# Kernel tuning notes

Measured on AMD Instinct MI355X. Metric: run time of the kernel, lower is better.

## Reference

```python
import jax, jax.numpy as jnp
import numpy as np

N = 128
# maskDD = full 128x128 (all True); maskL = strictly lower triangular.
# torch's M[:, mask] = entries fills True positions in row-major order,
# which matches np.tril_indices / nonzero ordering.
_L_ROWS, _L_COLS = np.tril_indices(N, -1)  # 8128 entries


def setup_inputs() -> dict:
    key = jax.random.key(0)
    k1, k2, k3 = jax.random.split(key, 3)
    B = 2048
    DD_entries = jax.random.normal(k1, (B, N * N), dtype=jnp.float32)
    L_entries = jax.random.normal(k2, (B, _L_ROWS.size), dtype=jnp.float32) * 0.05
    scale = jax.random.uniform(k3, (1,), dtype=jnp.float32, minval=0.1, maxval=0.5)
    return {"DD_entries": DD_entries, "L_entries": L_entries, "scale": scale}


def reference(DD_entries, L_entries, scale):
    B = DD_entries.shape[0]
    dtype = DD_entries.dtype
    # reconstruct_mat with full mask -> plain reshape
    DD = DD_entries.reshape(B, N, N)
    # reconstruct_mat with strictly-lower-triangular mask (scatter), then * scale
    eps = jnp.zeros((B, N, N), dtype=dtype).at[:, _L_ROWS, _L_COLS].set(L_entries)
    L = eps * scale + jnp.eye(N, dtype=dtype)  # epsilon*scale + I
    LL = L @ jnp.swapaxes(L, -1, -2)           # L L^H (real -> L L^T)
    P = LL @ DD                                 # preconditioned matrix [B,N,N]
    S = jnp.linalg.svd(P, compute_uv=False)    # singular values, descending
    cond = S[..., 0] / S[..., -1]
    return jnp.mean(cond, axis=0)
```

## Files before the change

### kernel.cpp

```cpp
#include <hip/hip_runtime.h>

#define N 128
#define PAD2 129
#define NL 8128
#define POWER_IT 10
#define INV_IT 3
#define INV_WAVES 8
#define NTHREADS 1024

#define NDBL (16512 + 128 + 24 + 24 + 16)
#define SMEM_BYTES (NDBL * 8 + 2 * 143 * 16)
#define XI(j) ((j) + ((j) >> 3))

static __device__ __forceinline__ float hashf(unsigned x) {
    x ^= 2747636419u; x *= 2654435769u; x ^= x >> 16;
    x *= 2654435769u; x ^= x >> 16; x *= 2654435769u;
    return ((float)(x >> 8)) * (1.0f / 16777216.0f) - 0.5f;
}
static __device__ __forceinline__ double readlane_d(double x, int lane) {
    int lo = __builtin_amdgcn_readlane(__double2loint(x), lane);
    int hi = __builtin_amdgcn_readlane(__double2hiint(x), lane);
    return __hiloint2double(hi, lo);
}

static __device__ __forceinline__ void cholInvC(const double* Gp, double* C) {
    double g[4][4];
    int c = 0;
    #pragma unroll
    for (int a = 0; a < 4; ++a)
        #pragma unroll
        for (int b2 = a; b2 < 4; ++b2) { g[a][b2] = Gp[c]; g[b2][a] = Gp[c]; ++c; }
    double R[4][4];
    #pragma unroll
    for (int i = 0; i < 4; ++i) {
        double d = g[i][i];
        #pragma unroll
        for (int m = 0; m < 4; ++m) if (m < i) d -= R[m][i] * R[m][i];
        d = sqrt(fmax(d, 1e-300));
        R[i][i] = d;
        #pragma unroll
        for (int j = 0; j < 4; ++j) if (j > i) {
            double v = g[i][j];
            #pragma unroll
            for (int m = 0; m < 4; ++m) if (m < i) v -= R[m][i] * R[m][j];
            R[i][j] = v / d;
        }
    }
    #pragma unroll
    for (int j = 3; j >= 0; --j) {
        C[j*4 + j] = 1.0 / R[j][j];
        #pragma unroll
        for (int i = 3; i >= 0; --i) if (i < j) {
            double v = 0.0;
            #pragma unroll
            for (int m = 0; m < 4; ++m) if (m > i && m <= j) v += R[i][m] * C[m*4 + j];
            C[i*4 + j] = -v / R[i][i];
        }
        #pragma unroll
        for (int i = 0; i < 4; ++i) if (i > j) C[i*4 + j] = 0.0;
    }
}

static __device__ __forceinline__ double jacobi4_lmax(const double* Gp) {
    double g[4][4];
    int c = 0;
    #pragma unroll
    for (int a = 0; a < 4; ++a)
        #pragma unroll
        for (int b2 = a; b2 < 4; ++b2) { g[a][b2] = Gp[c]; g[b2][a] = Gp[c]; ++c; }
    #pragma unroll
    for (int sweep = 0; sweep < 6; ++sweep) {
        #pragma unroll
        for (int p = 0; p < 3; ++p) {
            #pragma unroll
            for (int q = p + 1; q < 4; ++q) {
                double apq = g[p][q];
                double tau = (g[q][q] - g[p][p]) / (2.0 * apq);
                double t = (tau >= 0.0 ? 1.0 : -1.0) / (fabs(tau) + sqrt(1.0 + tau * tau));
                if (fabs(apq) < 1e-280) t = 0.0;
                double cc = 1.0 / sqrt(1.0 + t * t);
                double ss = t * cc;
                #pragma unroll
                for (int r = 0; r < 4; ++r) {
                    double grp = g[r][p], grq = g[r][q];
                    g[r][p] = cc * grp - ss * grq;
                    g[r][q] = ss * grp + cc * grq;
                }
                #pragma unroll
                for (int r = 0; r < 4; ++r) {
                    double gpr = g[p][r], gqr = g[q][r];
                    g[p][r] = cc * gpr - ss * gqr;
                    g[q][r] = ss * gpr + cc * gqr;
                }
            }
        }
    }
    return fmax(fmax(g[0][0], g[1][1]), fmax(g[2][2], g[3][3]));
}

static __device__ __forceinline__ void cholqr2_d(double ya[2], double yb[2]) {
    double g00 = ya[0]*ya[0] + yb[0]*yb[0];
    double g01 = ya[0]*ya[1] + yb[0]*yb[1];
    double g11 = ya[1]*ya[1] + yb[1]*yb[1];
    #pragma unroll
    for (int o = 32; o > 0; o >>= 1) {
        g00 += __shfl_xor(g00, o);
        g01 += __shfl_xor(g01, o);
        g11 += __shfl_xor(g11, o);
    }
    double r00 = sqrt(fmax(g00, 1e-300));
    double r01 = g01 / r00;
    double r11 = sqrt(fmax(g11 - r01 * r01, fabs(g11) * 1e-26 + 1e-300));
    double c00 = 1.0 / r00, c11 = 1.0 / r11;
    double c01 = -r01 * c00 * c11;
    double a0 = ya[0]*c00,             b0 = yb[0]*c00;
    double a1 = ya[0]*c01 + ya[1]*c11, b1 = yb[0]*c01 + yb[1]*c11;
    ya[0] = a0; yb[0] = b0; ya[1] = a1; yb[1] = b1;
}

template<int MODE>
static __device__ __forceinline__ void sweep4(const double* __restrict__ Ad,
                                              const float4* __restrict__ Xin,
                                              float4* __restrict__ Xout,
                                              int pr, int pc) {
    float a0 = 0.f, a1 = 0.f, a2 = 0.f, a3 = 0.f;
    #pragma unroll
    for (int t = 0; t < 16; ++t) {
        int j = pc + (t << 3);
        float a = (MODE < 2) ? (float)Ad[pr * PAD2 + j] : (float)Ad[j * PAD2 + pr];
        bool keep = (MODE == 0) ? (j >= pr) : (MODE == 1) ? (j < pr)
                  : (MODE == 2) ? (j > pr)  : (j <= pr);
        a = keep ? a : 0.f;
        float4 xv = Xin[XI(j)];
        a0 += a * xv.x; a1 += a * xv.y; a2 += a * xv.z; a3 += a * xv.w;
    }
    a0 += __shfl_xor(a0, 1); a0 += __shfl_xor(a0, 2); a0 += __shfl_xor(a0, 4);
    a1 += __shfl_xor(a1, 1); a1 += __shfl_xor(a1, 2); a1 += __shfl_xor(a1, 4);
    a2 += __shfl_xor(a2, 1); a2 += __shfl_xor(a2, 2); a2 += __shfl_xor(a2, 4);
    a3 += __shfl_xor(a3, 1); a3 += __shfl_xor(a3, 2); a3 += __shfl_xor(a3, 4);
    if (pc == 0) {
        float4 o = make_float4(a0, a1, a2, a3);
        if (MODE == 1 || MODE == 2) {
            float4 iv = Xin[XI(pr)];
            o.x += iv.x; o.y += iv.y; o.z += iv.z; o.w += iv.w;
        }
        Xout[XI(pr)] = o;
    }
}

__global__ __launch_bounds__(NTHREADS)
__attribute__((amdgpu_waves_per_eu(4, 4)))
void cond_kernel(const float* __restrict__ DD, const float* __restrict__ LE,
                 const float* __restrict__ SCL, double* __restrict__ conds)
{
    extern __shared__ char smraw[];
    double* Ad    = (double*)smraw;
    double* dinvd = Ad + N * PAD2;
    double* dmisc = dinvd + 128;
    double* dred  = dmisc + 24;
    double* dG    = dred + 24;
    float4* fX4   = (float4*)(Ad + NDBL);
    float4* fW4   = fX4 + 143;

    const int tid = threadIdx.x;
    const int b   = blockIdx.x;
    const int wid = tid >> 6;
    const int l   = tid & 63;
    const int rB  = l + 64;
    const double s = (double)SCL[0];
    const float* dd = DD + (size_t)b * (N * N);
    const float* le = LE + (size_t)b * NL;

    for (int t = tid; t < (N * N) / 4; t += NTHREADS) {
        float4 dv = reinterpret_cast<const float4*>(dd)[t];
        int elem = t * 4;
        int i = elem >> 7, j = elem & 127;
        double* dst = &Ad[i * PAD2 + j];
        dst[0] = (double)dv.x; dst[1] = (double)dv.y;
        dst[2] = (double)dv.z; dst[3] = (double)dv.w;
    }
    __syncthreads();

    const int pr_ = tid >> 5;
    const int pc_ = tid & 31;

    for (int KB = 0; KB < N; KB += 32) {
        const int k = KB + pr_;
        double acc[4];
        #pragma unroll
        for (int e = 0; e < 4; ++e) acc[e] = 0.0;
        int off = (KB + 1) * KB / 2 + k;
        #pragma unroll 4
        for (int i = KB + 1; i < N; ++i) {
            int offs = (i > k) ? off : 0;
            float lef = le[offs];
            double lv = (i > k) ? (double)lef : 0.0;
            #pragma unroll
            for (int e = 0; e < 4; ++e) acc[e] += lv * Ad[i * PAD2 + pc_ + 32 * e];
            off += i;
        }
        __syncthreads();
        #pragma unroll
        for (int e = 0; e < 4; ++e) Ad[k * PAD2 + pc_ + 32 * e] += s * acc[e];
        __syncthreads();
    }

    for (int IB = N - 32; IB >= 0; IB -= 32) {
        const int i = IB + pr_;
        const float* er = le + i * (i - 1) / 2;
        double acc[4];
        #pragma unroll
        for (int e = 0; e < 4; ++e) acc[e] = 0.0;
        #pragma unroll 4
        for (int m = 0; m < IB + 32; ++m) {
            int mm = (m < i) ? m : 0;
            float lef = er[mm];
            double lv = (m < i) ? (double)lef : 0.0;
            #pragma unroll
            for (int e = 0; e < 4; ++e) acc[e] += lv * Ad[m * PAD2 + pc_ + 32 * e];
        }
        __syncthreads();
        #pragma unroll
        for (int e = 0; e < 4; ++e) Ad[i * PAD2 + pc_ + 32 * e] += s * acc[e];
        __syncthreads();
    }

    for (int k = 0; k < N - 1; ++k) {
        if (wid == 0) {
            float v0 = (l >= k) ? (float)fabs(Ad[l * PAD2 + k]) : -1.0f;
            float v1 = (rB >= k) ? (float)fabs(Ad[rB * PAD2 + k]) : -1.0f;
            float vm = v0; int im = l;
            if (v1 > vm) { vm = v1; im = rB; }
            #pragma unroll
            for (int o = 32; o > 0; o >>= 1) {
                float ov = __shfl_xor(vm, o);
                int   oi = __shfl_xor(im, o);
                if (ov > vm) { vm = ov; im = oi; }
            }
            if (l == 0) dinvd[k] = 1.0 / Ad[im * PAD2 + k];
            if (im != k) {
                double t0 = Ad[k * PAD2 + l];
                Ad[k * PAD2 + l] = Ad[im * PAD2 + l];
                Ad[im * PAD2 + l] = t0;
                double t1 = Ad[k * PAD2 + rB];
                Ad[k * PAD2 + rB] = Ad[im * PAD2 + rB];
                Ad[im * PAD2 + rB] = t1;
            }
        }
        __syncthreads();
        double invd = dinvd[k];
        int g32 = tid >> 5, l32 = tid & 31;
        double ukj[4];
        #pragma unroll
        for (int m2 = 0; m2 < 4; ++m2) {
            int j = k + 1 + l32 + 32 * m2;
            ukj[m2] = (j < N) ? Ad[k * PAD2 + j] : 0.0;
        }
        #pragma unroll 2
        for (int i = k + 1 + g32; i < N; i += 32) {
            double lik = Ad[i * PAD2 + k] * invd;
            if (l32 == 0) Ad[i * PAD2 + k] = lik;
            #pragma unroll
            for (int m2 = 0; m2 < 4; ++m2) {
                int j = k + 1 + l32 + 32 * m2;
                if (j < N) Ad[i * PAD2 + j] -= lik * ukj[m2];
            }
        }
        __syncthreads();
    }
    if (tid == 0) dinvd[N - 1] = 1.0 / Ad[(N - 1) * PAD2 + (N - 1)];
    __syncthreads();

    {
        const int pr = tid >> 3;
        const int pc = tid & 7;
        if (tid < 128) {
            float4 xv;
            xv.x = hashf(13u + (unsigned)tid * 7919u);
            xv.y = hashf(14u + (unsigned)tid * 7919u);
            xv.z = hashf(15u + (unsigned)tid * 7919u);
            xv.w = hashf(16u + (unsigned)tid * 7919u);
            fX4[XI(tid)] = xv;
        }
        __syncthreads();

        float4* Xin = fX4;
        float4* Xout = fW4;
        const int wv = tid >> 6;

        for (int it = 0; it < POWER_IT; ++it) {
            sweep4<0>(Ad, Xin, Xout, pr, pc); __syncthreads();
            { float4* tmp = Xin; Xin = Xout; Xout = tmp; }
            sweep4<1>(Ad, Xin, Xout, pr, pc); __syncthreads();
            { float4* tmp = Xin; Xin = Xout; Xout = tmp; }
            sweep4<2>(Ad, Xin, Xout, pr, pc); __syncthreads();
            { float4* tmp = Xin; Xin = Xout; Xout = tmp; }
            sweep4<3>(Ad, Xin, Xout, pr, pc); __syncthreads();
            { float4* tmp = Xin; Xin = Xout; Xout = tmp; }

            if ((it & 1) == 0) {
                if (tid < 128) {
                    float4 x = Xin[XI(tid)];
                    float n0 = x.x*x.x, n1 = x.y*x.y, n2 = x.z*x.z, n3 = x.w*x.w;
                    #pragma unroll
                    for (int o = 32; o > 0; o >>= 1) {
                        n0 += __shfl_xor(n0, o); n1 += __shfl_xor(n1, o);
                        n2 += __shfl_xor(n2, o); n3 += __shfl_xor(n3, o);
                    }
                    if (l == 0) {
                        dred[wv*4 + 0] = (double)n0; dred[wv*4 + 1] = (double)n1;
                        dred[wv*4 + 2] = (double)n2; dred[wv*4 + 3] = (double)n3;
                    }
                }
                __syncthreads();
                if (tid < 128) {
                    float i0 = rsqrtf((float)(dred[0] + dred[4]) + 1e-30f);
                    float i1 = rsqrtf((float)(dred[1] + dred[5]) + 1e-30f);
                    float i2 = rsqrtf((float)(dred[2] + dred[6]) + 1e-30f);
                    float i3 = rsqrtf((float)(dred[3] + dred[7]) + 1e-30f);
                    float4 x = Xin[XI(tid)];
                    x.x *= i0; x.y *= i1; x.z *= i2; x.w *= i3;
                    Xin[XI(tid)] = x;
                }
                __syncthreads();
            } else {
                if (tid < 128) {
                    float4 x = Xin[XI(tid)];
                    float xs[4] = {x.x, x.y, x.z, x.w};
                    double p[10];
                    { int c = 0;
                      #pragma unroll
                      for (int v = 0; v < 4; ++v)
                          #pragma unroll
                          for (int w2 = v; w2 < 4; ++w2) { p[c] = (double)xs[v] * xs[w2]; ++c; } }
                    #pragma unroll
                    for (int o = 32; o > 0; o >>= 1)
                        #pragma unroll
                        for (int c2 = 0; c2 < 10; ++c2) p[c2] += __shfl_xor(p[c2], o);
                    if (l == 0)
                        for (int c2 = 0; c2 < 10; ++c2) dred[wv*10 + c2] = p[c2];
                }
                __syncthreads();
                if (tid == 0) {
                    double Gp[10];
                    #pragma unroll
                    for (int c2 = 0; c2 < 10; ++c2) Gp[c2] = dred[c2] + dred[10 + c2];
                    cholInvC(Gp, dG);
                }
                __syncthreads();
                if (tid < 128) {
                    float4 x = Xin[XI(tid)];
                    double x0 = x.x, x1 = x.y, x2 = x.z, x3 = x.w;
                    float n0 = (float)(dG[0]*x0);
                    float n1 = (float)(dG[1]*x0 + dG[5]*x1);
                    float n2 = (float)(dG[2]*x0 + dG[6]*x1 + dG[10]*x2);
                    float n3 = (float)(dG[3]*x0 + dG[7]*x1 + dG[11]*x2 + dG[15]*x3);
                    Xin[XI(tid)] = make_float4(n0, n1, n2, n3);
                }
                __syncthreads();
            }
        }

        sweep4<0>(Ad, Xin, Xout, pr, pc); __syncthreads();
        { float4* tmp = Xin; Xin = Xout; Xout = tmp; }
        sweep4<1>(Ad, Xin, Xout, pr, pc); __syncthreads();
        { float4* tmp = Xin; Xin = Xout; Xout = tmp; }
        if (tid < 128) {
            float4 x = Xin[XI(tid)];
            float xs[4] = {x.x, x.y, x.z, x.w};
            double p[10];
            { int c = 0;
              #pragma unroll
              for (int v = 0; v < 4; ++v)
                  #pragma unroll
                  for (int w2 = v; w2 < 4; ++w2) { p[c] = (double)xs[v] * xs[w2]; ++c; } }
            #pragma unroll
            for (int o = 32; o > 0; o >>= 1)
                #pragma unroll
                for (int c2 = 0; c2 < 10; ++c2) p[c2] += __shfl_xor(p[c2], o);
            if (l == 0)
                for (int c2 = 0; c2 < 10; ++c2) dred[wv*10 + c2] = p[c2];
        }
        __syncthreads();
        if (tid == 0) {
            double Gp[10];
            #pragma unroll
            for (int c2 = 0; c2 < 10; ++c2) Gp[c2] = dred[c2] + dred[10 + c2];
            dmisc[0] = jacobi4_lmax(Gp);
        }
    }

    if (wid < INV_WAVES) {
        unsigned seed = 2654435761u * (unsigned)(wid + 1) + 12345u;
        double ya[2], yb[2];
        #pragma unroll
        for (int v = 0; v < 2; ++v) {
            ya[v] = (double)hashf(seed + (unsigned)(v * 337 + l * 101 + 7));
            yb[v] = (double)hashf(seed + (unsigned)(v * 337 + rB * 101 + 7));
        }
        for (int it = 0; it < INV_IT; ++it) {
            #pragma unroll 4
            for (int i = 0; i < 64; ++i) {
                double invd = dinvd[i];
                double u0 = Ad[i * PAD2 + l];
                double u1 = Ad[i * PAD2 + rB];
                bool up0 = (l > i);
                #pragma unroll
                for (int v = 0; v < 2; ++v) {
                    double av = readlane_d(ya[v], i) * invd;
                    double upd = ya[v] - u0 * av;
                    ya[v] = (l == i) ? av : (up0 ? upd : ya[v]);
                    yb[v] -= u1 * av;
                }
            }
            #pragma unroll 4
            for (int i2 = 0; i2 < 64; ++i2) {
                double invd = dinvd[64 + i2];
                double u1 = Ad[(64 + i2) * PAD2 + rB];
                bool up1 = (l > i2);
                #pragma unroll
                for (int v = 0; v < 2; ++v) {
                    double av = readlane_d(yb[v], i2) * invd;
                    double upd = yb[v] - u1 * av;
                    yb[v] = (l == i2) ? av : (up1 ? upd : yb[v]);
                }
            }
            #pragma unroll 4
            for (int j2 = 63; j2 >= 0; --j2) {
                int j = 64 + j2;
                double L0 = Ad[j * PAD2 + l];
                double L1 = Ad[j * PAD2 + rB];
                bool m1 = (l < j2);
                #pragma unroll
                for (int v = 0; v < 2; ++v) {
                    double bv = readlane_d(yb[v], j2);
                    ya[v] -= L0 * bv;
                    double upd = yb[v] - L1 * bv;
                    yb[v] = m1 ? upd : yb[v];
                }
            }
            #pragma unroll 4
            for (int j = 63; j >= 1; --j) {
                double L0 = Ad[j * PAD2 + l];
                bool m0 = (l < j);
                #pragma unroll
                for (int v = 0; v < 2; ++v) {
                    double bv = readlane_d(ya[v], j);
                    double upd = ya[v] - L0 * bv;
                    ya[v] = m0 ? upd : ya[v];
                }
            }
            #pragma unroll 4
            for (int j = 0; j < 64; ++j) {
                double La0 = Ad[l * PAD2 + j];
                double La1 = Ad[rB * PAD2 + j];
                bool m0 = (l > j);
                #pragma unroll
                for (int v = 0; v < 2; ++v) {
                    double cv = readlane_d(ya[v], j);
                    double upd = ya[v] - La0 * cv;
                    ya[v] = m0 ? upd : ya[v];
                    yb[v] -= La1 * cv;
                }
            }
            #pragma unroll 4
            for (int j2 = 0; j2 < 64; ++j2) {
                double La1 = Ad[rB * PAD2 + 64 + j2];
                bool m1 = (l > j2);
                #pragma unroll
                for (int v = 0; v < 2; ++v) {
                    double cv = readlane_d(yb[v], j2);
                    double upd = yb[v] - La1 * cv;
                    yb[v] = m1 ? upd : yb[v];
                }
            }
            #pragma unroll 4
            for (int i2 = 63; i2 >= 0; --i2) {
                int i = 64 + i2;
                double invd = dinvd[i];
                double U0 = Ad[l * PAD2 + i];
                double U1 = Ad[rB * PAD2 + i];
                bool m1 = (l < i2);
                #pragma unroll
                for (int v = 0; v < 2; ++v) {
                    double xv = readlane_d(yb[v], i2) * invd;
                    ya[v] -= U0 * xv;
                    double upd = yb[v] - U1 * xv;
                    yb[v] = (l == i2) ? xv : (m1 ? upd : yb[v]);
                }
            }
            #pragma unroll 4
            for (int i = 63; i >= 0; --i) {
                double invd = dinvd[i];
                double U0 = Ad[l * PAD2 + i];
                bool m0 = (l < i);
                #pragma unroll
                for (int v = 0; v < 2; ++v) {
                    double xv = readlane_d(ya[v], i) * invd;
                    double upd = ya[v] - U0 * xv;
                    ya[v] = (l == i) ? xv : (m0 ? upd : ya[v]);
                }
            }
            cholqr2_d(ya, yb);
        }
        double t0[2] = {0, 0}, t1[2] = {0, 0};
        #pragma unroll 4
        for (int j = 0; j < 64; ++j) {
            double u0 = Ad[l * PAD2 + j];
            u0 = (j >= l) ? u0 : 0.0;
            #pragma unroll
            for (int v = 0; v < 2; ++v) { double yj = readlane_d(ya[v], j); t0[v] += u0 * yj; }
        }
        #pragma unroll 4
        for (int j2 = 0; j2 < 64; ++j2) {
            int j = 64 + j2;
            double u0 = Ad[l * PAD2 + j];
            double u1 = Ad[rB * PAD2 + j];
            u1 = (j2 >= l) ? u1 : 0.0;
            #pragma unroll
            for (int v = 0; v < 2; ++v) {
                double yj = readlane_d(yb[v], j2);
                t0[v] += u0 * yj; t1[v] += u1 * yj;
            }
        }
        double z0[2] = {t0[0], t0[1]}, z1[2] = {t1[0], t1[1]};
        #pragma unroll 4
        for (int j = 0; j < 64; ++j) {
            double L0 = Ad[l * PAD2 + j];
            L0 = (j < l) ? L0 : 0.0;
            double L1 = Ad[rB * PAD2 + j];
            #pragma unroll
            for (int v = 0; v < 2; ++v) {
                double tj = readlane_d(t0[v], j);
                z0[v] += L0 * tj; z1[v] += L1 * tj;
            }
        }
        #pragma unroll 4
        for (int j2 = 0; j2 < 64; ++j2) {
            double L1 = Ad[rB * PAD2 + 64 + j2];
            L1 = (j2 < l) ? L1 : 0.0;
            #pragma unroll
            for (int v = 0; v < 2; ++v) {
                double tj = readlane_d(t1[v], j2);
                z1[v] += L1 * tj;
            }
        }
        double g00 = z0[0]*z0[0] + z1[0]*z1[0];
        double g01 = z0[0]*z0[1] + z1[0]*z1[1];
        double g11 = z0[1]*z0[1] + z1[1]*z1[1];
        #pragma unroll
        for (int o = 32; o > 0; o >>= 1) {
            g00 += __shfl_xor(g00, o);
            g01 += __shfl_xor(g01, o);
            g11 += __shfl_xor(g11, o);
        }
        double dif = g00 - g11;
        double lmin = 0.5 * ((g00 + g11) - sqrt(dif * dif + 4.0 * g01 * g01));
        if (l == 0) dmisc[1 + wid] = lmin;
    }
    __syncthreads();
    if (tid == 0) {
        double lmin = dmisc[1];
        #pragma unroll
        for (int w2 = 2; w2 <= INV_WAVES; ++w2) lmin = fmin(lmin, dmisc[w2]);
        conds[b] = sqrt(fmax(dmisc[0], 0.0) / fmax(lmin, 1e-290));
    }
}

__global__ void reduce_kernel(const double* __restrict__ conds, float* __restrict__ out, int B) {
    __shared__ double sred[4];
    int tid = threadIdx.x;
    double acc = 0.0;
    for (int i = tid; i < B; i += 256) acc += conds[i];
    #pragma unroll
    for (int o = 32; o > 0; o >>= 1) acc += __shfl_xor(acc, o);
    if ((tid & 63) == 0) sred[tid >> 6] = acc;
    __syncthreads();
    if (tid == 0) out[0] = (float)((sred[0] + sred[1] + sred[2] + sred[3]) / (double)B);
}

extern "C" void kernel_launch(void* const* d_in, const int* in_sizes, int n_in,
                              void* d_out, int out_size, void* d_ws, size_t ws_size,
                              hipStream_t stream) {
    const float* DD = (const float*)d_in[0];
    const float* LE = (const float*)d_in[1];
    const float* SC = (const float*)d_in[2];
    float* out = (float*)d_out;
    int B = in_sizes[0] / (N * N);
    double* conds = (double*)d_ws;

    static_assert(SMEM_BYTES <= 160 * 1024, "LDS budget");
    (void)hipFuncSetAttribute((const void*)cond_kernel,
                              hipFuncAttributeMaxDynamicSharedMemorySize, (int)SMEM_BYTES);
    hipLaunchKernelGGL(cond_kernel, dim3(B), dim3(NTHREADS), SMEM_BYTES, stream, DD, LE, SC, conds);
    hipLaunchKernelGGL(reduce_kernel, dim3(1), dim3(256), 0, stream, conds, out, B);
}
```

Before: 4.309 ms.

## Run power iteration and inverse iteration concurrently on split wave groups

Waves 8-15 now run the power-iteration sweeps for the largest singular value while waves 0-7 run inverse iteration for the smallest, in lockstep chunks separated by block barriers, where before the two phases ran one after the other. The power sweeps are remapped to 4 lanes per row with 32 contiguous columns each, since only 512 threads are left for them. The power iteration count drops from 10 to 8, trading some convergence accuracy for fewer steps. Splitting the work into chunks adds barriers, and the two halves have different chunk costs, so each barrier waits for the slower side.

```diff
diff --git a/kernel.cpp b/kernel.cpp
--- a/kernel.cpp
+++ b/kernel.cpp
@@ -3,10 +3,12 @@
 #define N 128
 #define PAD2 129
 #define NL 8128
-#define POWER_IT 10
+#define POWER_IT 8
 #define INV_IT 3
-#define INV_WAVES 8
 #define NTHREADS 1024
+
+#define PCHUNKS (7 * POWER_IT + 4)
+#define ICHUNKS (9 * INV_IT + 5)
 
 #define NDBL (16512 + 128 + 24 + 24 + 16)
 #define SMEM_BYTES (NDBL * 8 + 2 * 143 * 16)
@@ -119,14 +121,15 @@
 }
 
 template<int MODE>
-static __device__ __forceinline__ void sweep4(const double* __restrict__ Ad,
+static __device__ __forceinline__ void sweepP(const double* __restrict__ Ad,
                                               const float4* __restrict__ Xin,
                                               float4* __restrict__ Xout,
                                               int pr, int pc) {
+    const int jbase = pc << 5;
     float a0 = 0.f, a1 = 0.f, a2 = 0.f, a3 = 0.f;
     #pragma unroll
-    for (int t = 0; t < 16; ++t) {
-        int j = pc + (t << 3);
+    for (int t = 0; t < 32; ++t) {
+        int j = jbase + t;
         float a = (MODE < 2) ? (float)Ad[pr * PAD2 + j] : (float)Ad[j * PAD2 + pr];
         bool keep = (MODE == 0) ? (j >= pr) : (MODE == 1) ? (j < pr)
                   : (MODE == 2) ? (j > pr)  : (j <= pr);
@@ -134,10 +137,10 @@
         float4 xv = Xin[XI(j)];
         a0 += a * xv.x; a1 += a * xv.y; a2 += a * xv.z; a3 += a * xv.w;
     }
-    a0 += __shfl_xor(a0, 1); a0 += __shfl_xor(a0, 2); a0 += __shfl_xor(a0, 4);
-    a1 += __shfl_xor(a1, 1); a1 += __shfl_xor(a1, 2); a1 += __shfl_xor(a1, 4);
-    a2 += __shfl_xor(a2, 1); a2 += __shfl_xor(a2, 2); a2 += __shfl_xor(a2, 4);
-    a3 += __shfl_xor(a3, 1); a3 += __shfl_xor(a3, 2); a3 += __shfl_xor(a3, 4);
+    a0 += __shfl_xor(a0, 1); a0 += __shfl_xor(a0, 2);
+    a1 += __shfl_xor(a1, 1); a1 += __shfl_xor(a1, 2);
+    a2 += __shfl_xor(a2, 1); a2 += __shfl_xor(a2, 2);
+    a3 += __shfl_xor(a3, 1); a3 += __shfl_xor(a3, 2);
     if (pc == 0) {
         float4 o = make_float4(a0, a1, a2, a3);
         if (MODE == 1 || MODE == 2) {
@@ -269,300 +272,314 @@
         __syncthreads();
     }
     if (tid == 0) dinvd[N - 1] = 1.0 / Ad[(N - 1) * PAD2 + (N - 1)];
-    __syncthreads();
-
-    {
-        const int pr = tid >> 3;
-        const int pc = tid & 7;
-        if (tid < 128) {
-            float4 xv;
-            xv.x = hashf(13u + (unsigned)tid * 7919u);
-            xv.y = hashf(14u + (unsigned)tid * 7919u);
-            xv.z = hashf(15u + (unsigned)tid * 7919u);
-            xv.w = hashf(16u + (unsigned)tid * 7919u);
-            fX4[XI(tid)] = xv;
-        }
-        __syncthreads();
-
-        float4* Xin = fX4;
-        float4* Xout = fW4;
-        const int wv = tid >> 6;
-
-        for (int it = 0; it < POWER_IT; ++it) {
-            sweep4<0>(Ad, Xin, Xout, pr, pc); __syncthreads();
-            { float4* tmp = Xin; Xin = Xout; Xout = tmp; }
-            sweep4<1>(Ad, Xin, Xout, pr, pc); __syncthreads();
-            { float4* tmp = Xin; Xin = Xout; Xout = tmp; }
-            sweep4<2>(Ad, Xin, Xout, pr, pc); __syncthreads();
-            { float4* tmp = Xin; Xin = Xout; Xout = tmp; }
-            sweep4<3>(Ad, Xin, Xout, pr, pc); __syncthreads();
-            { float4* tmp = Xin; Xin = Xout; Xout = tmp; }
-
-            if ((it & 1) == 0) {
-                if (tid < 128) {
-                    float4 x = Xin[XI(tid)];
-                    float n0 = x.x*x.x, n1 = x.y*x.y, n2 = x.z*x.z, n3 = x.w*x.w;
-                    #pragma unroll
-                    for (int o = 32; o > 0; o >>= 1) {
-                        n0 += __shfl_xor(n0, o); n1 += __shfl_xor(n1, o);
-                        n2 += __shfl_xor(n2, o); n3 += __shfl_xor(n3, o);
-                    }
-                    if (l == 0) {
-                        dred[wv*4 + 0] = (double)n0; dred[wv*4 + 1] = (double)n1;
-                        dred[wv*4 + 2] = (double)n2; dred[wv*4 + 3] = (double)n3;
-                    }
-                }
-                __syncthreads();
-                if (tid < 128) {
-                    float i0 = rsqrtf((float)(dred[0] + dred[4]) + 1e-30f);
-                    float i1 = rsqrtf((float)(dred[1] + dred[5]) + 1e-30f);
-                    float i2 = rsqrtf((float)(dred[2] + dred[6]) + 1e-30f);
-                    float i3 = rsqrtf((float)(dred[3] + dred[7]) + 1e-30f);
-                    float4 x = Xin[XI(tid)];
-                    x.x *= i0; x.y *= i1; x.z *= i2; x.w *= i3;
-                    Xin[XI(tid)] = x;
-                }
-                __syncthreads();
-            } else {
-                if (tid < 128) {
-                    float4 x = Xin[XI(tid)];
-                    float xs[4] = {x.x, x.y, x.z, x.w};
-                    double p[10];
-                    { int c = 0;
-                      #pragma unroll
-                      for (int v = 0; v < 4; ++v)
-                          #pragma unroll
-                          for (int w2 = v; w2 < 4; ++w2) { p[c] = (double)xs[v] * xs[w2]; ++c; } }
-                    #pragma unroll
-                    for (int o = 32; o > 0; o >>= 1)
-                        #pragma unroll
-                        for (int c2 = 0; c2 < 10; ++c2) p[c2] += __shfl_xor(p[c2], o);
-                    if (l == 0)
-                        for (int c2 = 0; c2 < 10; ++c2) dred[wv*10 + c2] = p[c2];
-                }
-                __syncthreads();
-                if (tid == 0) {
-                    double Gp[10];
-                    #pragma unroll
-                    for (int c2 = 0; c2 < 10; ++c2) Gp[c2] = dred[c2] + dred[10 + c2];
-                    cholInvC(Gp, dG);
-                }
-                __syncthreads();
-                if (tid < 128) {
-                    float4 x = Xin[XI(tid)];
-                    double x0 = x.x, x1 = x.y, x2 = x.z, x3 = x.w;
-                    float n0 = (float)(dG[0]*x0);
-                    float n1 = (float)(dG[1]*x0 + dG[5]*x1);
-                    float n2 = (float)(dG[2]*x0 + dG[6]*x1 + dG[10]*x2);
-                    float n3 = (float)(dG[3]*x0 + dG[7]*x1 + dG[11]*x2 + dG[15]*x3);
-                    Xin[XI(tid)] = make_float4(n0, n1, n2, n3);
-                }
-                __syncthreads();
-            }
-        }
-
-        sweep4<0>(Ad, Xin, Xout, pr, pc); __syncthreads();
-        { float4* tmp = Xin; Xin = Xout; Xout = tmp; }
-        sweep4<1>(Ad, Xin, Xout, pr, pc); __syncthreads();
-        { float4* tmp = Xin; Xin = Xout; Xout = tmp; }
-        if (tid < 128) {
-            float4 x = Xin[XI(tid)];
-            float xs[4] = {x.x, x.y, x.z, x.w};
-            double p[10];
-            { int c = 0;
-              #pragma unroll
-              for (int v = 0; v < 4; ++v)
-                  #pragma unroll
-                  for (int w2 = v; w2 < 4; ++w2) { p[c] = (double)xs[v] * xs[w2]; ++c; } }
-            #pragma unroll
-            for (int o = 32; o > 0; o >>= 1)
-                #pragma unroll
-                for (int c2 = 0; c2 < 10; ++c2) p[c2] += __shfl_xor(p[c2], o);
-            if (l == 0)
-                for (int c2 = 0; c2 < 10; ++c2) dred[wv*10 + c2] = p[c2];
-        }
-        __syncthreads();
-        if (tid == 0) {
-            double Gp[10];
-            #pragma unroll
-            for (int c2 = 0; c2 < 10; ++c2) Gp[c2] = dred[c2] + dred[10 + c2];
-            dmisc[0] = jacobi4_lmax(Gp);
-        }
-    }
-
-    if (wid < INV_WAVES) {
+
+    const int tid2 = tid - 512;
+    const int prP  = tid2 >> 2;
+    const int pcP  = tid2 & 3;
+    const int wv2  = tid2 >> 6;
+
+    if (wid >= 8 && tid2 < 128) {
+        float4 xv;
+        xv.x = hashf(13u + (unsigned)tid2 * 7919u);
+        xv.y = hashf(14u + (unsigned)tid2 * 7919u);
+        xv.z = hashf(15u + (unsigned)tid2 * 7919u);
+        xv.w = hashf(16u + (unsigned)tid2 * 7919u);
+        fX4[XI(tid2)] = xv;
+    }
+    double ya[2] = {0, 0}, yb[2] = {0, 0};
+    double rt0[2] = {0, 0}, rt1[2] = {0, 0}, rz0[2] = {0, 0}, rz1[2] = {0, 0};
+    if (wid < 8) {
         unsigned seed = 2654435761u * (unsigned)(wid + 1) + 12345u;
-        double ya[2], yb[2];
         #pragma unroll
         for (int v = 0; v < 2; ++v) {
             ya[v] = (double)hashf(seed + (unsigned)(v * 337 + l * 101 + 7));
             yb[v] = (double)hashf(seed + (unsigned)(v * 337 + rB * 101 + 7));
         }
-        for (int it = 0; it < INV_IT; ++it) {
-            #pragma unroll 4
-            for (int i = 0; i < 64; ++i) {
-                double invd = dinvd[i];
-                double u0 = Ad[i * PAD2 + l];
-                double u1 = Ad[i * PAD2 + rB];
-                bool up0 = (l > i);
-                #pragma unroll
-                for (int v = 0; v < 2; ++v) {
-                    double av = readlane_d(ya[v], i) * invd;
-                    double upd = ya[v] - u0 * av;
-                    ya[v] = (l == i) ? av : (up0 ? upd : ya[v]);
-                    yb[v] -= u1 * av;
+    }
+    __syncthreads();
+
+    for (int c = 0; c < PCHUNKS; ++c) {
+        if (wid >= 8) {
+            if (c < 7 * POWER_IT) {
+                const int itp = c / 7, ph = c % 7;
+                if      (ph == 0) sweepP<0>(Ad, fX4, fW4, prP, pcP);
+                else if (ph == 1) sweepP<1>(Ad, fW4, fX4, prP, pcP);
+                else if (ph == 2) sweepP<2>(Ad, fX4, fW4, prP, pcP);
+                else if (ph == 3) sweepP<3>(Ad, fW4, fX4, prP, pcP);
+                else if (ph == 4) {
+                    if (tid2 < 128) {
+                        float4 x = fX4[XI(tid2)];
+                        if ((itp & 1) == 0) {
+                            float n0 = x.x*x.x, n1 = x.y*x.y, n2 = x.z*x.z, n3 = x.w*x.w;
+                            #pragma unroll
+                            for (int o = 32; o > 0; o >>= 1) {
+                                n0 += __shfl_xor(n0, o); n1 += __shfl_xor(n1, o);
+                                n2 += __shfl_xor(n2, o); n3 += __shfl_xor(n3, o);
+                            }
+                            if (l == 0) {
+                                dred[wv2*4 + 0] = (double)n0; dred[wv2*4 + 1] = (double)n1;
+                                dred[wv2*4 + 2] = (double)n2; dred[wv2*4 + 3] = (double)n3;
+                            }
+                        } else {
+                            float xs[4] = {x.x, x.y, x.z, x.w};
+                            double p[10];
+                            { int cc = 0;
+                              #pragma unroll
+                              for (int v = 0; v < 4; ++v)
+                                  #pragma unroll
+                                  for (int w2 = v; w2 < 4; ++w2) { p[cc] = (double)xs[v] * xs[w2]; ++cc; } }
+                            #pragma unroll
+                            for (int o = 32; o > 0; o >>= 1)
+                                #pragma unroll
+                                for (int c2 = 0; c2 < 10; ++c2) p[c2] += __shfl_xor(p[c2], o);
+                            if (l == 0)
+                                for (int c2 = 0; c2 < 10; ++c2) dred[wv2*10 + c2] = p[c2];
+                        }
+                    }
+                } else if (ph == 5) {
+                    if ((itp & 1) == 1 && tid == 512) {
+                        double Gp[10];
+                        #pragma unroll
+                        for (int c2 = 0; c2 < 10; ++c2) Gp[c2] = dred[c2] + dred[10 + c2];
+                        cholInvC(Gp, dG);
+                    }
+                } else {
+                    if (tid2 < 128) {
+                        float4 x = fX4[XI(tid2)];
+                        if ((itp & 1) == 0) {
+                            float i0 = rsqrtf((float)(dred[0] + dred[4]) + 1e-30f);
+                            float i1 = rsqrtf((float)(dred[1] + dred[5]) + 1e-30f);
+                            float i2 = rsqrtf((float)(dred[2] + dred[6]) + 1e-30f);
+                            float i3 = rsqrtf((float)(dred[3] + dred[7]) + 1e-30f);
+                            x.x *= i0; x.y *= i1; x.z *= i2; x.w *= i3;
+                            fX4[XI(tid2)] = x;
+                        } else {
+                            double x0 = x.x, x1 = x.y, x2 = x.z, x3 = x.w;
+                            float n0 = (float)(dG[0]*x0);
+                            float n1 = (float)(dG[1]*x0 + dG[5]*x1);
+                            float n2 = (float)(dG[2]*x0 + dG[6]*x1 + dG[10]*x2);
+                            float n3 = (float)(dG[3]*x0 + dG[7]*x1 + dG[11]*x2 + dG[15]*x3);
+                            fX4[XI(tid2)] = make_float4(n0, n1, n2, n3);
+                        }
+                    }
+                }
+            } else {
+                const int rc = c - 7 * POWER_IT;
+                if      (rc == 0) sweepP<0>(Ad, fX4, fW4, prP, pcP);
+                else if (rc == 1) sweepP<1>(Ad, fW4, fX4, prP, pcP);
+                else if (rc == 2) {
+                    if (tid2 < 128) {
+                        float4 x = fX4[XI(tid2)];
+                        float xs[4] = {x.x, x.y, x.z, x.w};
+                        double p[10];
+                        { int cc = 0;
+                          #pragma unroll
+                          for (int v = 0; v < 4; ++v)
+                              #pragma unroll
+                              for (int w2 = v; w2 < 4; ++w2) { p[cc] = (double)xs[v] * xs[w2]; ++cc; } }
+                        #pragma unroll
+                        for (int o = 32; o > 0; o >>= 1)
+                            #pragma unroll
+                            for (int c2 = 0; c2 < 10; ++c2) p[c2] += __shfl_xor(p[c2], o);
+                        if (l == 0)
+                            for (int c2 = 0; c2 < 10; ++c2) dred[wv2*10 + c2] = p[c2];
+                    }
+                } else {
+                    if (tid == 512) {
+                        double Gp[10];
+                        #pragma unroll
+                        for (int c2 = 0; c2 < 10; ++c2) Gp[c2] = dred[c2] + dred[10 + c2];
+                        dmisc[0] = jacobi4_lmax(Gp);
+                    }
                 }
             }
-            #pragma unroll 4
-            for (int i2 = 0; i2 < 64; ++i2) {
-                double invd = dinvd[64 + i2];
-                double u1 = Ad[(64 + i2) * PAD2 + rB];
-                bool up1 = (l > i2);
-                #pragma unroll
-                for (int v = 0; v < 2; ++v) {
-                    double av = readlane_d(yb[v], i2) * invd;
-                    double upd = yb[v] - u1 * av;
-                    yb[v] = (l == i2) ? av : (up1 ? upd : yb[v]);
+        } else {
+            if (c < 9 * INV_IT) {
+                const int ph = c % 9;
+                if (ph == 0) {
+                    #pragma unroll 4
+                    for (int i = 0; i < 64; ++i) {
+                        double invd = dinvd[i];
+                        double u0 = Ad[i * PAD2 + l];
+                        double u1 = Ad[i * PAD2 + rB];
+                        bool up0 = (l > i);
+                        #pragma unroll
+                        for (int v = 0; v < 2; ++v) {
+                            double av = readlane_d(ya[v], i) * invd;
+                            double upd = ya[v] - u0 * av;
+                            ya[v] = (l == i) ? av : (up0 ? upd : ya[v]);
+                            yb[v] -= u1 * av;
+                        }
+                    }
+                } else if (ph == 1) {
+                    #pragma unroll 4
+                    for (int i2 = 0; i2 < 64; ++i2) {
+                        double invd = dinvd[64 + i2];
+                        double u1 = Ad[(64 + i2) * PAD2 + rB];
+                        bool up1 = (l > i2);
+                        #pragma unroll
+                        for (int v = 0; v < 2; ++v) {
+                            double av = readlane_d(yb[v], i2) * invd;
+                            double upd = yb[v] - u1 * av;
+                            yb[v] = (l == i2) ? av : (up1 ? upd : yb[v]);
+                        }
+                    }
+                } else if (ph == 2) {
+                    #pragma unroll 4
+                    for (int j2 = 63; j2 >= 0; --j2) {
+                        int j = 64 + j2;
+                        double L0 = Ad[j * PAD2 + l];
+                        double L1 = Ad[j * PAD2 + rB];
+                        bool m1 = (l < j2);
+                        #pragma unroll
+                        for (int v = 0; v < 2; ++v) {
+                            double bv = readlane_d(yb[v], j2);
+                            ya[v] -= L0 * bv;
+                            double upd = yb[v] - L1 * bv;
+                            yb[v] = m1 ? upd : yb[v];
+                        }
+                    }
+                } else if (ph == 3) {
+                    #pragma unroll 4
+                    for (int j = 63; j >= 1; --j) {
+                        double L0 = Ad[j * PAD2 + l];
+                        bool m0 = (l < j);
+                        #pragma unroll
+                        for (int v = 0; v < 2; ++v) {
+                            double bv = readlane_d(ya[v], j);
+                            double upd = ya[v] - L0 * bv;
+                            ya[v] = m0 ? upd : ya[v];
+                        }
+                    }
+                } else if (ph == 4) {
+                    #pragma unroll 4
+                    for (int j = 0; j < 64; ++j) {
+                        double La0 = Ad[l * PAD2 + j];
+                        double La1 = Ad[rB * PAD2 + j];
+                        bool m0 = (l > j);
+                        #pragma unroll
+                        for (int v = 0; v < 2; ++v) {
+                            double cv = readlane_d(ya[v], j);
+                            double upd = ya[v] - La0 * cv;
+                            ya[v] = m0 ? upd : ya[v];
+                            yb[v] -= La1 * cv;
+                        }
+                    }
+                } else if (ph == 5) {
+                    #pragma unroll 4
+                    for (int j2 = 0; j2 < 64; ++j2) {
+                        double La1 = Ad[rB * PAD2 + 64 + j2];
+                        bool m1 = (l > j2);
+                        #pragma unroll
+                        for (int v = 0; v < 2; ++v) {
+                            double cv = readlane_d(yb[v], j2);
+                            double upd = yb[v] - La1 * cv;
+                            yb[v] = m1 ? upd : yb[v];
+                        }
+                    }
+                } else if (ph == 6) {
+                    #pragma unroll 4
+                    for (int i2 = 63; i2 >= 0; --i2) {
+                        int i = 64 + i2;
+                        double invd = dinvd[i];
+                        double U0 = Ad[l * PAD2 + i];
+                        double U1 = Ad[rB * PAD2 + i];
+                        bool m1 = (l < i2);
+                        #pragma unroll
+                        for (int v = 0; v < 2; ++v) {
+                            double xv = readlane_d(yb[v], i2) * invd;
+                            ya[v] -= U0 * xv;
+                            double upd = yb[v] - U1 * xv;
+                            yb[v] = (l == i2) ? xv : (m1 ? upd : yb[v]);
+                        }
+                    }
+                } else if (ph == 7) {
+                    #pragma unroll 4
+                    for (int i = 63; i >= 0; --i) {
+                        double invd = dinvd[i];
+                        double U0 = Ad[l * PAD2 + i];
+                        bool m0 = (l < i);
+                        #pragma unroll
+                        for (int v = 0; v < 2; ++v) {
+                            double xv = readlane_d(ya[v], i) * invd;
+                            double upd = ya[v] - U0 * xv;
+                            ya[v] = (l == i) ? xv : (m0 ? upd : ya[v]);
+                        }
+                    }
+                } else {
+                    cholqr2_d(ya, yb);
+                }
+            } else if (c < ICHUNKS) {
+                const int rc = c - 9 * INV_IT;
+                if (rc == 0) {
+                    #pragma unroll 4
+                    for (int j = 0; j < 64; ++j) {
+                        double u0 = Ad[l * PAD2 + j];
+                        u0 = (j >= l) ? u0 : 0.0;
+                        #pragma unroll
+                        for (int v = 0; v < 2; ++v) { double yj = readlane_d(ya[v], j); rt0[v] += u0 * yj; }
+                    }
+                } else if (rc == 1) {
+                    #pragma unroll 4
+                    for (int j2 = 0; j2 < 64; ++j2) {
+                        int j = 64 + j2;
+                        double u0 = Ad[l * PAD2 + j];
+                        double u1 = Ad[rB * PAD2 + j];
+                        u1 = (j2 >= l) ? u1 : 0.0;
+                        #pragma unroll
+                        for (int v = 0; v < 2; ++v) {
+                            double yj = readlane_d(yb[v], j2);
+                            rt0[v] += u0 * yj; rt1[v] += u1 * yj;
+                        }
+                    }
+                } else if (rc == 2) {
+                    #pragma unroll
+                    for (int v = 0; v < 2; ++v) { rz0[v] = rt0[v]; rz1[v] = rt1[v]; }
+                    #pragma unroll 4
+                    for (int j = 0; j < 64; ++j) {
+                        double L0 = Ad[l * PAD2 + j];
+                        L0 = (j < l) ? L0 : 0.0;
+                        double L1 = Ad[rB * PAD2 + j];
+                        #pragma unroll
+                        for (int v = 0; v < 2; ++v) {
+                            double tj = readlane_d(rt0[v], j);
+                            rz0[v] += L0 * tj; rz1[v] += L1 * tj;
+                        }
+                    }
+                } else if (rc == 3) {
+                    #pragma unroll 4
+                    for (int j2 = 0; j2 < 64; ++j2) {
+                        double L1 = Ad[rB * PAD2 + 64 + j2];
+                        L1 = (j2 < l) ? L1 : 0.0;
+                        #pragma unroll
+                        for (int v = 0; v < 2; ++v) {
+                            double tj = readlane_d(rt1[v], j2);
+                            rz1[v] += L1 * tj;
+                        }
+                    }
+                } else {
+                    double g00 = rz0[0]*rz0[0] + rz1[0]*rz1[0];
+                    double g01 = rz0[0]*rz0[1] + rz1[0]*rz1[1];
+                    double g11 = rz0[1]*rz0[1] + rz1[1]*rz1[1];
+                    #pragma unroll
+                    for (int o = 32; o > 0; o >>= 1) {
+                        g00 += __shfl_xor(g00, o);
+                        g01 += __shfl_xor(g01, o);
+                        g11 += __shfl_xor(g11, o);
+                    }
+                    double dif = g00 - g11;
+                    double lmin = 0.5 * ((g00 + g11) - sqrt(dif * dif + 4.0 * g01 * g01));
+                    if (l == 0) dmisc[1 + wid] = lmin;
                 }
             }
-            #pragma unroll 4
-            for (int j2 = 63; j2 >= 0; --j2) {
-                int j = 64 + j2;
-                double L0 = Ad[j * PAD2 + l];
-                double L1 = Ad[j * PAD2 + rB];
-                bool m1 = (l < j2);
-                #pragma unroll
-                for (int v = 0; v < 2; ++v) {
-                    double bv = readlane_d(yb[v], j2);
-                    ya[v] -= L0 * bv;
-                    double upd = yb[v] - L1 * bv;
-                    yb[v] = m1 ? upd : yb[v];
-                }
-            }
-            #pragma unroll 4
-            for (int j = 63; j >= 1; --j) {
-                double L0 = Ad[j * PAD2 + l];
-                bool m0 = (l < j);
-                #pragma unroll
-                for (int v = 0; v < 2; ++v) {
-                    double bv = readlane_d(ya[v], j);
-                    double upd = ya[v] - L0 * bv;
-                    ya[v] = m0 ? upd : ya[v];
-                }
-            }
-            #pragma unroll 4
-            for (int j = 0; j < 64; ++j) {
-                double La0 = Ad[l * PAD2 + j];
-                double La1 = Ad[rB * PAD2 + j];
-                bool m0 = (l > j);
-                #pragma unroll
-                for (int v = 0; v < 2; ++v) {
-                    double cv = readlane_d(ya[v], j);
-                    double upd = ya[v] - La0 * cv;
-                    ya[v] = m0 ? upd : ya[v];
-                    yb[v] -= La1 * cv;
-                }
-            }
-            #pragma unroll 4
-            for (int j2 = 0; j2 < 64; ++j2) {
-                double La1 = Ad[rB * PAD2 + 64 + j2];
-                bool m1 = (l > j2);
-                #pragma unroll
-                for (int v = 0; v < 2; ++v) {
-                    double cv = readlane_d(yb[v], j2);
-                    double upd = yb[v] - La1 * cv;
-                    yb[v] = m1 ? upd : yb[v];
-                }
-            }
-            #pragma unroll 4
-            for (int i2 = 63; i2 >= 0; --i2) {
-                int i = 64 + i2;
-                double invd = dinvd[i];
-                double U0 = Ad[l * PAD2 + i];
-                double U1 = Ad[rB * PAD2 + i];
-                bool m1 = (l < i2);
-                #pragma unroll
-                for (int v = 0; v < 2; ++v) {
-                    double xv = readlane_d(yb[v], i2) * invd;
-                    ya[v] -= U0 * xv;
-                    double upd = yb[v] - U1 * xv;
-                    yb[v] = (l == i2) ? xv : (m1 ? upd : yb[v]);
-                }
-            }
-            #pragma unroll 4
-            for (int i = 63; i >= 0; --i) {
-                double invd = dinvd[i];
-                double U0 = Ad[l * PAD2 + i];
-                bool m0 = (l < i);
-                #pragma unroll
-                for (int v = 0; v < 2; ++v) {
-                    double xv = readlane_d(ya[v], i) * invd;
-                    double upd = ya[v] - U0 * xv;
-                    ya[v] = (l == i) ? xv : (m0 ? upd : ya[v]);
-                }
-            }
-            cholqr2_d(ya, yb);
-        }
-        double t0[2] = {0, 0}, t1[2] = {0, 0};
-        #pragma unroll 4
-        for (int j = 0; j < 64; ++j) {
-            double u0 = Ad[l * PAD2 + j];
-            u0 = (j >= l) ? u0 : 0.0;
-            #pragma unroll
-            for (int v = 0; v < 2; ++v) { double yj = readlane_d(ya[v], j); t0[v] += u0 * yj; }
-        }
-        #pragma unroll 4
-        for (int j2 = 0; j2 < 64; ++j2) {
-            int j = 64 + j2;
-            double u0 = Ad[l * PAD2 + j];
-            double u1 = Ad[rB * PAD2 + j];
-            u1 = (j2 >= l) ? u1 : 0.0;
-            #pragma unroll
-            for (int v = 0; v < 2; ++v) {
-                double yj = readlane_d(yb[v], j2);
-                t0[v] += u0 * yj; t1[v] += u1 * yj;
-            }
-        }
-        double z0[2] = {t0[0], t0[1]}, z1[2] = {t1[0], t1[1]};
-        #pragma unroll 4
-        for (int j = 0; j < 64; ++j) {
-            double L0 = Ad[l * PAD2 + j];
-            L0 = (j < l) ? L0 : 0.0;
-            double L1 = Ad[rB * PAD2 + j];
-            #pragma unroll
-            for (int v = 0; v < 2; ++v) {
-                double tj = readlane_d(t0[v], j);
-                z0[v] += L0 * tj; z1[v] += L1 * tj;
-            }
-        }
-        #pragma unroll 4
-        for (int j2 = 0; j2 < 64; ++j2) {
-            double L1 = Ad[rB * PAD2 + 64 + j2];
-            L1 = (j2 < l) ? L1 : 0.0;
-            #pragma unroll
-            for (int v = 0; v < 2; ++v) {
-                double tj = readlane_d(t1[v], j2);
-                z1[v] += L1 * tj;
-            }
-        }
-        double g00 = z0[0]*z0[0] + z1[0]*z1[0];
-        double g01 = z0[0]*z0[1] + z1[0]*z1[1];
-        double g11 = z0[1]*z0[1] + z1[1]*z1[1];
-        #pragma unroll
-        for (int o = 32; o > 0; o >>= 1) {
-            g00 += __shfl_xor(g00, o);
-            g01 += __shfl_xor(g01, o);
-            g11 += __shfl_xor(g11, o);
-        }
-        double dif = g00 - g11;
-        double lmin = 0.5 * ((g00 + g11) - sqrt(dif * dif + 4.0 * g01 * g01));
-        if (l == 0) dmisc[1 + wid] = lmin;
-    }
-    __syncthreads();
+        }
+        __syncthreads();
+    }
+
     if (tid == 0) {
         double lmin = dmisc[1];
         #pragma unroll
-        for (int w2 = 2; w2 <= INV_WAVES; ++w2) lmin = fmin(lmin, dmisc[w2]);
+        for (int w2 = 2; w2 <= 8; ++w2) lmin = fmin(lmin, dmisc[w2]);
         conds[b] = sqrt(fmax(dmisc[0], 0.0) / fmax(lmin, 1e-290));
     }
 }
@@ -589,6 +606,7 @@
     int B = in_sizes[0] / (N * N);
     double* conds = (double*)d_ws;
 
+    static_assert(ICHUNKS <= PCHUNKS, "inverse must fit under power window");
     static_assert(SMEM_BYTES <= 160 * 1024, "LDS budget");
     (void)hipFuncSetAttribute((const void*)cond_kernel,
                               hipFuncAttributeMaxDynamicSharedMemorySize, (int)SMEM_BYTES);
```

New measurement: 6.029 ms. +39.9%, slower.
